# Kernel optimization log

Measured on AMD Instinct MI355X. Metric: run time of the kernel, lower is better.

## Reference

```python
import jax, jax.numpy as jnp
import numpy as np

N = 100000   # nodes
E = 1200000  # edges
NIN, EIN = 6, 1
HID, L, H = 64, 3, 4
D = HID // H  # 16 per-head dim


def setup_inputs() -> dict:
    key = jax.random.key(0)
    ks = jax.random.split(key, 20)
    r = lambda k, shape: (jax.random.normal(k, shape, dtype=jnp.float32) * 0.1)
    inp = {
        "x": jax.random.normal(ks[0], (N, NIN), dtype=jnp.float32),
        "edge_index": jax.random.randint(ks[1], (2, E), 0, N, dtype=jnp.int64),
        "edge_attr": jax.random.normal(ks[2], (E, EIN), dtype=jnp.float32),
        # node encoder (Linear-ReLU-Linear)
        "w_ne1": r(ks[3], (NIN, HID)), "b_ne1": jnp.zeros((HID,), jnp.float32),
        "w_ne2": r(ks[4], (HID, HID)), "b_ne2": jnp.zeros((HID,), jnp.float32),
        # edge encoder (Linear)
        "w_ee": r(ks[5], (EIN, HID)), "b_ee": jnp.zeros((HID,), jnp.float32),
        # stacked GAT layers (PyG GATConv w/ edge features, concat heads)
        "w_gat": r(ks[6], (L, HID, HID)),      # node lin per layer
        "w_eg": r(ks[7], (L, HID, HID)),       # edge lin per layer
        "att_src": r(ks[8], (L, H, D)),
        "att_dst": r(ks[9], (L, H, D)),
        "att_edge": r(ks[10], (L, H, D)),
        "b_gat": jnp.zeros((L, HID), jnp.float32),
        # per-layer LayerNorm
        "ln_g": jnp.ones((L, HID), jnp.float32),
        "ln_b": jnp.zeros((L, HID), jnp.float32),
        # output projection
        "w_out": r(ks[11], (HID, HID)), "b_out": jnp.zeros((HID,), jnp.float32),
    }
    return inp


def _layernorm(x, g, b, eps=1e-5):
    m = jnp.mean(x, axis=-1, keepdims=True)
    v = jnp.mean(jnp.square(x - m), axis=-1, keepdims=True)
    return (x - m) * jax.lax.rsqrt(v + eps) * g + b


def reference(x, edge_index, edge_attr, w_ne1, b_ne1, w_ne2, b_ne2, w_ee, b_ee,
              w_gat, w_eg, att_src, att_dst, att_edge, b_gat, ln_g, ln_b,
              w_out, b_out):
    n = x.shape[0]
    src, dst = edge_index[0], edge_index[1]
    # encode nodes / edges
    h = jax.nn.relu(x @ w_ne1 + b_ne1) @ w_ne2 + b_ne2          # [N, HID]
    e = edge_attr @ w_ee + b_ee                                  # [E, HID]
    num_layers = w_gat.shape[0]
    for l in range(num_layers):
        hw = (h @ w_gat[l]).reshape(n, H, D)                     # [N,H,D]
        ew = (e @ w_eg[l]).reshape(-1, H, D)                     # [E,H,D]
        a_s = jnp.sum(hw * att_src[l], axis=-1)                  # [N,H]
        a_d = jnp.sum(hw * att_dst[l], axis=-1)                  # [N,H]
        a_e = jnp.sum(ew * att_edge[l], axis=-1)                 # [E,H]
        score = jax.nn.leaky_relu(a_s[src] + a_d[dst] + a_e, 0.2)  # [E,H]
        # softmax over incoming edges of each destination node
        smax = jax.ops.segment_max(score, dst, num_segments=n)
        ex = jnp.exp(score - smax[dst])
        den = jax.ops.segment_sum(ex, dst, num_segments=n)
        alpha = ex / (den[dst] + 1e-16)                          # [E,H]
        msg = alpha[:, :, None] * hw[src]                        # [E,H,D]
        agg = jax.ops.segment_sum(msg, dst, num_segments=n)      # [N,H,D]
        agg = agg.reshape(n, H * D) + b_gat[l]
        h = _layernorm(h + jax.nn.elu(agg), ln_g[l], ln_b[l])
    return h @ w_out + b_out
```

## Files before the change

kernel.cpp:

```cpp
#include <hip/hip_runtime.h>

#define NIN 6
#define HIDN 64
#define NHEAD 4
#define DEGPAD 5

__device__ __forceinline__ unsigned short f2bf(float f) {
    unsigned u = __float_as_uint(f);
    unsigned r = (u >> 16) & 1u;
    return (unsigned short)((u + 0x7fffu + r) >> 16);
}

__device__ __forceinline__ void mm64_plain_body(
    const float* __restrict__ src, const float* __restrict__ W,
    const float* __restrict__ bias, float* __restrict__ dst, int N,
    int wv0, int nw) {
    int j = threadIdx.x & 63;
    float Wc[HIDN];
#pragma unroll
    for (int k = 0; k < HIDN; k++) Wc[k] = W[k * HIDN + j];
    float bj = bias[j];
    for (int n0 = wv0; n0 < N; n0 += nw) {
        int n = __builtin_amdgcn_readfirstlane(n0);
        const float4* __restrict__ row = (const float4*)(src + (size_t)n * HIDN);
        float a0 = 0.f, a1 = 0.f, a2 = 0.f, a3 = 0.f;
#pragma unroll
        for (int kk = 0; kk < 16; kk++) {
            float4 r = row[kk];
            a0 += r.x * Wc[4 * kk];
            a1 += r.y * Wc[4 * kk + 1];
            a2 += r.z * Wc[4 * kk + 2];
            a3 += r.w * Wc[4 * kk + 3];
        }
        dst[(size_t)n * HIDN + j] = ((a0 + a1) + (a2 + a3)) + bj;
    }
}

__device__ __forceinline__ void mm64_attn_body(
    const float* __restrict__ src, const float* __restrict__ W,
    const float* __restrict__ att_s, const float* __restrict__ att_d,
    unsigned short* __restrict__ dst16,
    float* __restrict__ a_s, float* __restrict__ a_d, int N,
    int wv0, int nw) {
    int j = threadIdx.x & 63;
    float Wc[HIDN];
#pragma unroll
    for (int k = 0; k < HIDN; k++) Wc[k] = W[k * HIDN + j];
    float asj = att_s[j];
    float adj = att_d[j];
    for (int n0 = wv0; n0 < N; n0 += nw) {
        int n = __builtin_amdgcn_readfirstlane(n0);
        const float4* __restrict__ row = (const float4*)(src + (size_t)n * HIDN);
        float a0 = 0.f, a1 = 0.f, a2 = 0.f, a3 = 0.f;
#pragma unroll
        for (int kk = 0; kk < 16; kk++) {
            float4 r = row[kk];
            a0 += r.x * Wc[4 * kk];
            a1 += r.y * Wc[4 * kk + 1];
            a2 += r.z * Wc[4 * kk + 2];
            a3 += r.w * Wc[4 * kk + 3];
        }
        float acc = (a0 + a1) + (a2 + a3);
        dst16[(size_t)n * HIDN + j] = f2bf(acc);
        float ts = acc * asj;
        float td = acc * adj;
#pragma unroll
        for (int o = 8; o > 0; o >>= 1) {
            ts += __shfl_xor(ts, o);
            td += __shfl_xor(td, o);
        }
        if ((j & 15) == 0) {
            a_s[(size_t)n * NHEAD + (j >> 4)] = ts;
            a_d[(size_t)n * NHEAD + (j >> 4)] = td;
        }
    }
}

__global__ __launch_bounds__(256) void pre_kernel(
    const int* __restrict__ ei, unsigned* __restrict__ deg,
    unsigned* __restrict__ rank, int E,
    const float* __restrict__ x, const float* __restrict__ w1,
    const float* __restrict__ b1, float* __restrict__ hid, int N,
    const float* __restrict__ w_ee, const float* __restrict__ b_ee,
    const float* __restrict__ w_eg, const float* __restrict__ att_edge,
    float* __restrict__ c1, float* __restrict__ c0,
    int histBlocks, int encBlocks) {
    int b = blockIdx.x;
    if (b < histBlocks) {
        int e = b * 256 + threadIdx.x;
        if (e < E) rank[e] = atomicAdd(&deg[(size_t)ei[E + e] << DEGPAD], 1u);
        return;
    }
    b -= histBlocks;
    if (b < encBlocks) {
        int t = b * 256 + threadIdx.x;
        int n = t >> 6, j = t & 63;
        if (n >= N) return;
        float acc = b1[j];
#pragma unroll
        for (int i = 0; i < NIN; i++) acc += x[n * NIN + i] * w1[i * HIDN + j];
        hid[(size_t)n * HIDN + j] = acc > 0.f ? acc : 0.f;
        return;
    }
    int w = threadIdx.x >> 6, j = threadIdx.x & 63;
    for (int p = w; p < 12; p += 4) {
        int l = p >> 2, hh = p & 3;
        const float* wr = w_eg + l * 4096 + j * 64 + hh * 16;
        const float* ae = att_edge + l * 64 + hh * 16;
        float wj = 0.f;
#pragma unroll
        for (int d = 0; d < 16; d++) wj += wr[d] * ae[d];
        float s1 = w_ee[j] * wj;
        float s0 = b_ee[j] * wj;
#pragma unroll
        for (int o = 32; o > 0; o >>= 1) {
            s1 += __shfl_xor(s1, o);
            s0 += __shfl_xor(s0, o);
        }
        if (j == 0) { c1[l * 4 + hh] = s1; c0[l * 4 + hh] = s0; }
    }
}

__global__ __launch_bounds__(256) void mid_kernel(
    const unsigned* __restrict__ deg, unsigned* __restrict__ rp,
    unsigned* __restrict__ st, int N, int E,
    const float* __restrict__ src, const float* __restrict__ W,
    const float* __restrict__ bias, float* __restrict__ dst,
    int scanBlocks, int mmWaves) {
    int b = blockIdx.x;
    if (b < scanBlocks) {
        __shared__ unsigned sm[256];
        __shared__ unsigned s_prefix;
        int t = threadIdx.x, i = b * 256 + t;
        unsigned v = (i < N) ? deg[(size_t)i << DEGPAD] : 0u;
        sm[t] = v;
        __syncthreads();
        unsigned xx = v;
        for (int o = 1; o < 256; o <<= 1) {
            unsigned add = (t >= o) ? sm[t - o] : 0u;
            __syncthreads();
            xx += add; sm[t] = xx;
            __syncthreads();
        }
        if (t == 255) {
            unsigned tag = (b == 0) ? (2u << 30) : (1u << 30);
            __hip_atomic_store(&st[b], tag | xx, __ATOMIC_RELEASE,
                               __HIP_MEMORY_SCOPE_AGENT);
        }
        if (b == 0) {
            if (t == 0) s_prefix = 0u;
        } else if (t < 64) {
            unsigned pfx = 0u;
            int base = b - 1;
            for (;;) {
                int j = base - t;
                unsigned s;
                for (;;) {
                    s = (j >= 0) ? __hip_atomic_load(&st[j], __ATOMIC_ACQUIRE,
                                                     __HIP_MEMORY_SCOPE_AGENT)
                                 : (2u << 30);
                    if (__all((s >> 30) != 0u)) break;
                }
                unsigned long long m2 = __ballot((s >> 30) == 2u);
                if (m2 != 0ull) {
                    int k = __ffsll(m2) - 1;
                    unsigned val = (t <= k) ? (s & 0x3fffffffu) : 0u;
#pragma unroll
                    for (int o = 32; o > 0; o >>= 1) val += __shfl_xor(val, o);
                    pfx += val;
                    break;
                } else {
                    unsigned val = (j >= 0) ? (s & 0x3fffffffu) : 0u;
#pragma unroll
                    for (int o = 32; o > 0; o >>= 1) val += __shfl_xor(val, o);
                    pfx += val;
                    base -= 64;
                }
            }
            if (t == 0) {
                s_prefix = pfx;
                __hip_atomic_store(&st[b], (2u << 30) | (pfx + sm[255]),
                                   __ATOMIC_RELEASE, __HIP_MEMORY_SCOPE_AGENT);
            }
        }
        __syncthreads();
        if (i < N) rp[i] = (xx - v) + s_prefix;
        if (i == N - 1) rp[N] = (unsigned)E;
        return;
    }
    int wv0 = ((b - scanBlocks) * 256 + threadIdx.x) >> 6;
    mm64_plain_body(src, W, bias, dst, N, wv0, mmWaves);
}

__global__ __launch_bounds__(256) void sca_kernel(
    const int* __restrict__ ei, const float* __restrict__ eattr,
    const unsigned* __restrict__ rp, const unsigned* __restrict__ rank,
    int2* __restrict__ eca, int E,
    const float* __restrict__ src, const float* __restrict__ W,
    const float* __restrict__ att_s, const float* __restrict__ att_d,
    unsigned short* __restrict__ dst16,
    float* __restrict__ a_s, float* __restrict__ a_d, int N,
    int scatBlocks, int mmWaves) {
    int b = blockIdx.x;
    if (b < scatBlocks) {
        int e = b * 256 + threadIdx.x;
        if (e >= E) return;
        int s = ei[e], d = ei[E + e];
        unsigned p = rp[d] + rank[e];
        eca[p] = make_int2(s, __float_as_int(eattr[e]));
        return;
    }
    int wv0 = ((b - scatBlocks) * 256 + threadIdx.x) >> 6;
    mm64_attn_body(src, W, att_s, att_d, dst16, a_s, a_d, N, wv0, mmWaves);
}

template <int MODE>
__global__ __launch_bounds__(256) void gat_fused_x_kernel(
    const unsigned* __restrict__ rp, const int2* __restrict__ eca,
    const unsigned short* __restrict__ hw16,
    const float* __restrict__ a_s, const float* __restrict__ a_d,
    const float* __restrict__ c1, const float* __restrict__ c0,
    float* __restrict__ h, const float* __restrict__ bg,
    const float* __restrict__ g, const float* __restrict__ b, int N,
    const float* __restrict__ Wnext,
    const float* __restrict__ att_s_w, const float* __restrict__ att_d_w,
    const float* __restrict__ bias_out,
    unsigned short* __restrict__ hw16_out,
    float* __restrict__ a_s_out, float* __restrict__ a_d_out,
    float* __restrict__ out) {
    __shared__ float WgL[4096];
    __shared__ float exl[4 * 272];
    __shared__ int srl[4 * 68];

    {
        const float4* __restrict__ Wn4 = (const float4*)Wnext;
        float4* WgL4 = (float4*)WgL;
        for (int i = threadIdx.x; i < 1024; i += 256) WgL4[i] = Wn4[i];
    }
    __syncthreads();

    int t = blockIdx.x * blockDim.x + threadIdx.x;
    int lane = t & 63;
    int q = lane >> 4;
    int l = lane & 15;
    int hd = l >> 2;
    int sub = l & 3;
    int n = ((t >> 6) << 2) + q;
    int wslot = (threadIdx.x >> 6);
    float* myex = exl + wslot * 272 + 68 * q;
    int* mysrc = srl + wslot * 68 + 17 * q;

    bool nv = n < N;
    unsigned beg = nv ? rp[n] : 0u;
    int deg = nv ? (int)(rp[n + 1] - beg) : 0;

    float4 ad4 = nv ? *(const float4*)(a_d + ((size_t)n << 2)) : make_float4(0, 0, 0, 0);
    float4 C1 = *(const float4*)c1;
    float4 C0 = *(const float4*)c0;

    int md = deg;
    md = max(md, __shfl_xor(md, 16));
    md = max(md, __shfl_xor(md, 32));
    int chunks = (md + 15) >> 4;

    const unsigned* __restrict__ hwp = (const unsigned*)hw16;
    unsigned loff = (unsigned)(l << 1);

    float ssum = 0.f;
    float ac0 = 0.f, ac1 = 0.f, ac2 = 0.f, ac3 = 0.f;

    for (int k = 0; k < chunks; k++) {
        int i = (k << 4) + l;
        bool act = i < deg;
        int2 ce = act ? eca[beg + i] : make_int2(0, 0);
        int src = ce.x;
        float ea = __int_as_float(ce.y);
        float4 as4 = act ? *(const float4*)(a_s + ((size_t)src << 2))
                         : make_float4(0, 0, 0, 0);
        float s0 = as4.x + ad4.x + ea * C1.x + C0.x;
        float s1 = as4.y + ad4.y + ea * C1.y + C0.y;
        float s2 = as4.z + ad4.z + ea * C1.z + C0.z;
        float s3 = as4.w + ad4.w + ea * C1.w + C0.w;
        s0 = s0 >= 0.f ? s0 : 0.2f * s0;
        s1 = s1 >= 0.f ? s1 : 0.2f * s1;
        s2 = s2 >= 0.f ? s2 : 0.2f * s2;
        s3 = s3 >= 0.f ? s3 : 0.2f * s3;
        float e0 = act ? __expf(s0) : 0.f;
        float e1 = act ? __expf(s1) : 0.f;
        float e2 = act ? __expf(s2) : 0.f;
        float e3 = act ? __expf(s3) : 0.f;
        *(float4*)(myex + (l << 2)) = make_float4(e0, e1, e2, e3);
        mysrc[l] = act ? (src << 5) : 0;

        float w0 = myex[(sub << 2) + hd];
        float w1 = myex[((sub + 4) << 2) + hd];
        float w2 = myex[((sub + 8) << 2) + hd];
        float w3 = myex[((sub + 12) << 2) + hd];
        float csum = (w0 + w1) + (w2 + w3);
        csum += __shfl_xor(csum, 1);
        csum += __shfl_xor(csum, 2);
        ssum += csum;

#pragma unroll
        for (int e = 0; e < 16; e++) {
            float w = myex[(e << 2) + hd];
            unsigned so = (unsigned)mysrc[e];
            uint2 uu = *(const uint2*)(hwp + (so + loff));
            ac0 += w * __uint_as_float(uu.x << 16);
            ac1 += w * __uint_as_float(uu.x & 0xffff0000u);
            ac2 += w * __uint_as_float(uu.y << 16);
            ac3 += w * __uint_as_float(uu.y & 0xffff0000u);
        }
    }

    float inv = 1.f / (ssum + 1e-16f);
    float4 bg4 = *(const float4*)(bg + (l << 2));
    float4 hv4 = nv ? *(const float4*)(h + (size_t)n * HIDN + (l << 2))
                    : make_float4(0, 0, 0, 0);

    float a0 = ac0 * inv + bg4.x;
    float a1 = ac1 * inv + bg4.y;
    float a2 = ac2 * inv + bg4.z;
    float a3 = ac3 * inv + bg4.w;
    a0 = a0 > 0.f ? a0 : (__expf(a0) - 1.f);
    a1 = a1 > 0.f ? a1 : (__expf(a1) - 1.f);
    a2 = a2 > 0.f ? a2 : (__expf(a2) - 1.f);
    a3 = a3 > 0.f ? a3 : (__expf(a3) - 1.f);
    float v0 = hv4.x + a0, v1 = hv4.y + a1, v2 = hv4.z + a2, v3 = hv4.w + a3;

    float s = (v0 + v1) + (v2 + v3);
    float sq = (v0 * v0 + v1 * v1) + (v2 * v2 + v3 * v3);
#pragma unroll
    for (int o = 8; o > 0; o >>= 1) {
        s += __shfl_xor(s, o);
        sq += __shfl_xor(sq, o);
    }
    float mean = s * (1.f / 64.f);
    float var = sq * (1.f / 64.f) - mean * mean;
    float rr = rsqrtf(var + 1e-5f);
    float4 g4 = *(const float4*)(g + (l << 2));
    float4 b4 = *(const float4*)(b + (l << 2));
    v0 = (v0 - mean) * rr * g4.x + b4.x;
    v1 = (v1 - mean) * rr * g4.y + b4.y;
    v2 = (v2 - mean) * rr * g4.z + b4.z;
    v3 = (v3 - mean) * rr * g4.w + b4.w;

    if (MODE == 0 && nv) {
        *(float4*)(h + (size_t)n * HIDN + (l << 2)) = make_float4(v0, v1, v2, v3);
    }

    float* stg = exl + wslot * 272;
    *(float4*)(stg + (q << 6) + (l << 2)) = make_float4(v0, v1, v2, v3);

    float4 A0 = make_float4(0, 0, 0, 0), A1 = make_float4(0, 0, 0, 0);
    float4 A2 = make_float4(0, 0, 0, 0), A3 = make_float4(0, 0, 0, 0);
#pragma unroll
    for (int kk = 0; kk < 16; kk++) {
        float4 hk = *(const float4*)(stg + (q << 6) + (kk << 2));
        const float* wr = WgL + (kk << 8) + (l << 2);
        float4 w0 = *(const float4*)(wr);
        float4 w1 = *(const float4*)(wr + 64);
        float4 w2 = *(const float4*)(wr + 128);
        float4 w3 = *(const float4*)(wr + 192);
        A0.x += hk.x * w0.x; A0.y += hk.x * w0.y; A0.z += hk.x * w0.z; A0.w += hk.x * w0.w;
        A1.x += hk.y * w1.x; A1.y += hk.y * w1.y; A1.z += hk.y * w1.z; A1.w += hk.y * w1.w;
        A2.x += hk.z * w2.x; A2.y += hk.z * w2.y; A2.z += hk.z * w2.z; A2.w += hk.z * w2.w;
        A3.x += hk.w * w3.x; A3.y += hk.w * w3.y; A3.z += hk.w * w3.z; A3.w += hk.w * w3.w;
    }
    float o0 = (A0.x + A1.x) + (A2.x + A3.x);
    float o1 = (A0.y + A1.y) + (A2.y + A3.y);
    float o2 = (A0.z + A1.z) + (A2.z + A3.z);
    float o3 = (A0.w + A1.w) + (A2.w + A3.w);

    if (MODE == 0) {
        if (nv) {
            ushort4 pk = make_ushort4(f2bf(o0), f2bf(o1), f2bf(o2), f2bf(o3));
            *(ushort4*)(hw16_out + (size_t)n * HIDN + (l << 2)) = pk;
        }
        float4 asw = *(const float4*)(att_s_w + (l << 2));
        float4 adw = *(const float4*)(att_d_w + (l << 2));
        float ts = (o0 * asw.x + o1 * asw.y) + (o2 * asw.z + o3 * asw.w);
        float td = (o0 * adw.x + o1 * adw.y) + (o2 * adw.z + o3 * adw.w);
        ts += __shfl_xor(ts, 1); ts += __shfl_xor(ts, 2);
        td += __shfl_xor(td, 1); td += __shfl_xor(td, 2);
        if (nv && (l & 3) == 0) {
            a_s_out[(size_t)n * NHEAD + (l >> 2)] = ts;
            a_d_out[(size_t)n * NHEAD + (l >> 2)] = td;
        }
    } else {
        if (nv) {
            float4 bo = *(const float4*)(bias_out + (l << 2));
            *(float4*)(out + (size_t)n * HIDN + (l << 2)) =
                make_float4(o0 + bo.x, o1 + bo.y, o2 + bo.z, o3 + bo.w);
        }
    }
}

extern "C" void kernel_launch(void* const* d_in, const int* in_sizes, int n_in,
                              void* d_out, int out_size, void* d_ws, size_t ws_size,
                              hipStream_t stream) {
    const float* x      = (const float*)d_in[0];
    const int*   ei     = (const int*)d_in[1];
    const float* eattr  = (const float*)d_in[2];
    const float* w_ne1  = (const float*)d_in[3];
    const float* b_ne1  = (const float*)d_in[4];
    const float* w_ne2  = (const float*)d_in[5];
    const float* b_ne2  = (const float*)d_in[6];
    const float* w_ee   = (const float*)d_in[7];
    const float* b_ee   = (const float*)d_in[8];
    const float* w_gat  = (const float*)d_in[9];
    const float* w_eg   = (const float*)d_in[10];
    const float* att_src= (const float*)d_in[11];
    const float* att_dst= (const float*)d_in[12];
    const float* att_edge=(const float*)d_in[13];
    const float* b_gat  = (const float*)d_in[14];
    const float* ln_g   = (const float*)d_in[15];
    const float* ln_b   = (const float*)d_in[16];
    const float* w_out  = (const float*)d_in[17];
    const float* b_out  = (const float*)d_in[18];

    const int N = in_sizes[0] / NIN;
    const int E = in_sizes[2];

    float* ws   = (float*)d_ws;
    float* h    = ws;
    float* hid  = h + (size_t)N * 64;
    unsigned short* hw16 = (unsigned short*)(hid + (size_t)N * 64);
    float* a_s  = (float*)(hw16 + (size_t)N * 64);
    float* a_d  = a_s + (size_t)N * 4;
    float* c1   = a_d + (size_t)N * 4;
    float* c0   = c1 + 12;
    int2*  eca  = (int2*)(c0 + 12);
    unsigned* rank = (unsigned*)(eca + (size_t)E);
    unsigned* deg  = rank + (size_t)E;
    unsigned* st   = deg + ((size_t)N << DEGPAD);
    unsigned* rp   = st + 1024;

    unsigned short* hw16b = (unsigned short*)hid;
    float* a_sb = (float*)(hw16b + (size_t)N * 64);
    float* a_db = a_sb + (size_t)N * 4;

    dim3 blk(256);
    int edgeBlocks = (E + 255) / 256;
    int encBlocks  = (int)(((size_t)N * 64 + 255) / 256);
    int quadBlocks = (int)(((size_t)((N + 3) / 4) * 64 + 255) / 256);
    int nodeBlocks = (N + 255) / 256;
    int mmBlocks = 2048;
    int mmWaves  = mmBlocks * 4;

    hipMemsetAsync(deg, 0, (((size_t)N << DEGPAD) + 1024) * sizeof(unsigned), stream);

    pre_kernel<<<edgeBlocks + encBlocks + 1, blk, 0, stream>>>(
        ei, deg, rank, E,
        x, w_ne1, b_ne1, hid, N,
        w_ee, b_ee, w_eg, att_edge, c1, c0,
        edgeBlocks, encBlocks);

    mid_kernel<<<nodeBlocks + mmBlocks, blk, 0, stream>>>(
        deg, rp, st, N, E, hid, w_ne2, b_ne2, h, nodeBlocks, mmWaves);

    sca_kernel<<<edgeBlocks + mmBlocks, blk, 0, stream>>>(
        ei, eattr, rp, rank, eca, E,
        h, w_gat, att_src, att_dst, hw16, a_s, a_d, N,
        edgeBlocks, mmWaves);

    gat_fused_x_kernel<0><<<quadBlocks, blk, 0, stream>>>(
        rp, eca, hw16, a_s, a_d, c1 + 0, c0 + 0,
        h, b_gat + 0, ln_g + 0, ln_b + 0, N,
        w_gat + (size_t)1 * 4096, att_src + 64, att_dst + 64, nullptr,
        hw16b, a_sb, a_db, nullptr);

    gat_fused_x_kernel<0><<<quadBlocks, blk, 0, stream>>>(
        rp, eca, hw16b, a_sb, a_db, c1 + 4, c0 + 4,
        h, b_gat + 64, ln_g + 64, ln_b + 64, N,
        w_gat + (size_t)2 * 4096, att_src + 2 * 64, att_dst + 2 * 64, nullptr,
        hw16, a_s, a_d, nullptr);

    gat_fused_x_kernel<1><<<quadBlocks, blk, 0, stream>>>(
        rp, eca, hw16, a_s, a_d, c1 + 8, c0 + 8,
        h, b_gat + 2 * 64, ln_g + 2 * 64, ln_b + 2 * 64, N,
        w_out, nullptr, nullptr, b_out,
        nullptr, nullptr, nullptr, (float*)d_out);
}
```

Before: 453.7 us.

## Bucket nodes by in-degree within each block to balance wave workloads

During the degree scan, each block of 256 nodes now builds a local counting sort of its nodes by degree bucket (ceil(deg/16), capped at 15) and writes a permutation. The three GAT layer kernels process nodes in that permuted order, so the four nodes sharing a wave have similar chunk counts and lanes spend less time idle waiting on the highest-degree node. The cost is an extra indirection load per node, shared-memory atomics and a serial bucket prefix in the scan, and scattered rather than contiguous accesses to per-node rows (h, a_d, rp, outputs).

```diff
diff --git a/kernel.cpp b/kernel.cpp
--- a/kernel.cpp
+++ b/kernel.cpp
@@ -123,7 +123,7 @@
 
 __global__ __launch_bounds__(256) void mid_kernel(
     const unsigned* __restrict__ deg, unsigned* __restrict__ rp,
-    unsigned* __restrict__ st, int N, int E,
+    unsigned* __restrict__ st, unsigned* __restrict__ perm, int N, int E,
     const float* __restrict__ src, const float* __restrict__ W,
     const float* __restrict__ bias, float* __restrict__ dst,
     int scanBlocks, int mmWaves) {
@@ -131,9 +131,11 @@
     if (b < scanBlocks) {
         __shared__ unsigned sm[256];
         __shared__ unsigned s_prefix;
+        __shared__ unsigned bh[16];
         int t = threadIdx.x, i = b * 256 + t;
         unsigned v = (i < N) ? deg[(size_t)i << DEGPAD] : 0u;
         sm[t] = v;
+        if (t < 16) bh[t] = 0u;
         __syncthreads();
         unsigned xx = v;
         for (int o = 1; o < 256; o <<= 1) {
@@ -147,6 +149,9 @@
             __hip_atomic_store(&st[b], tag | xx, __ATOMIC_RELEASE,
                                __HIP_MEMORY_SCOPE_AGENT);
         }
+        unsigned bucket = min(15u, (v + 15u) >> 4);
+        unsigned myrank = 0u;
+        if (i < N) myrank = atomicAdd(&bh[bucket], 1u);
         if (b == 0) {
             if (t == 0) s_prefix = 0u;
         } else if (t < 64) {
@@ -186,6 +191,12 @@
         __syncthreads();
         if (i < N) rp[i] = (xx - v) + s_prefix;
         if (i == N - 1) rp[N] = (unsigned)E;
+        if (t == 0) {
+            unsigned run = 0;
+            for (int bb = 0; bb < 16; bb++) { unsigned c = bh[bb]; bh[bb] = run; run += c; }
+        }
+        __syncthreads();
+        if (i < N) perm[b * 256 + bh[bucket] + myrank] = (unsigned)i;
         return;
     }
     int wv0 = ((b - scanBlocks) * 256 + threadIdx.x) >> 6;
@@ -217,6 +228,7 @@
 template <int MODE>
 __global__ __launch_bounds__(256) void gat_fused_x_kernel(
     const unsigned* __restrict__ rp, const int2* __restrict__ eca,
+    const unsigned* __restrict__ perm,
     const unsigned short* __restrict__ hw16,
     const float* __restrict__ a_s, const float* __restrict__ a_d,
     const float* __restrict__ c1, const float* __restrict__ c0,
@@ -245,12 +257,13 @@
     int l = lane & 15;
     int hd = l >> 2;
     int sub = l & 3;
-    int n = ((t >> 6) << 2) + q;
+    int slot = ((t >> 6) << 2) + q;
     int wslot = (threadIdx.x >> 6);
     float* myex = exl + wslot * 272 + 68 * q;
     int* mysrc = srl + wslot * 68 + 17 * q;
 
-    bool nv = n < N;
+    bool nv = slot < N;
+    int n = nv ? (int)perm[slot] : 0;
     unsigned beg = nv ? rp[n] : 0u;
     int deg = nv ? (int)(rp[n + 1] - beg) : 0;
 
@@ -290,7 +303,7 @@
         float e2 = act ? __expf(s2) : 0.f;
         float e3 = act ? __expf(s3) : 0.f;
         *(float4*)(myex + (l << 2)) = make_float4(e0, e1, e2, e3);
-        mysrc[l] = act ? (src << 5) : 0;
+        mysrc[l] = act ? src : 0;
 
         float w0 = myex[(sub << 2) + hd];
         float w1 = myex[((sub + 4) << 2) + hd];
@@ -304,8 +317,8 @@
 #pragma unroll
         for (int e = 0; e < 16; e++) {
             float w = myex[(e << 2) + hd];
-            unsigned so = (unsigned)mysrc[e];
-            uint2 uu = *(const uint2*)(hwp + (so + loff));
+            int so = mysrc[e];
+            uint2 uu = *(const uint2*)(hwp + (((unsigned)so << 5) + loff));
             ac0 += w * __uint_as_float(uu.x << 16);
             ac1 += w * __uint_as_float(uu.x & 0xffff0000u);
             ac2 += w * __uint_as_float(uu.y << 16);
@@ -435,6 +448,7 @@
     unsigned* deg  = rank + (size_t)E;
     unsigned* st   = deg + ((size_t)N << DEGPAD);
     unsigned* rp   = st + 1024;
+    unsigned* perm = rp + (size_t)N + 1;
 
     unsigned short* hw16b = (unsigned short*)hid;
     float* a_sb = (float*)(hw16b + (size_t)N * 64);
@@ -457,7 +471,7 @@
         edgeBlocks, encBlocks);
 
     mid_kernel<<<nodeBlocks + mmBlocks, blk, 0, stream>>>(
-        deg, rp, st, N, E, hid, w_ne2, b_ne2, h, nodeBlocks, mmWaves);
+        deg, rp, st, perm, N, E, hid, w_ne2, b_ne2, h, nodeBlocks, mmWaves);
 
     sca_kernel<<<edgeBlocks + mmBlocks, blk, 0, stream>>>(
         ei, eattr, rp, rank, eca, E,
@@ -465,19 +479,19 @@
         edgeBlocks, mmWaves);
 
     gat_fused_x_kernel<0><<<quadBlocks, blk, 0, stream>>>(
-        rp, eca, hw16, a_s, a_d, c1 + 0, c0 + 0,
+        rp, eca, perm, hw16, a_s, a_d, c1 + 0, c0 + 0,
         h, b_gat + 0, ln_g + 0, ln_b + 0, N,
         w_gat + (size_t)1 * 4096, att_src + 64, att_dst + 64, nullptr,
         hw16b, a_sb, a_db, nullptr);
 
     gat_fused_x_kernel<0><<<quadBlocks, blk, 0, stream>>>(
-        rp, eca, hw16b, a_sb, a_db, c1 + 4, c0 + 4,
+        rp, eca, perm, hw16b, a_sb, a_db, c1 + 4, c0 + 4,
         h, b_gat + 64, ln_g + 64, ln_b + 64, N,
         w_gat + (size_t)2 * 4096, att_src + 2 * 64, att_dst + 2 * 64, nullptr,
         hw16, a_s, a_d, nullptr);
 
     gat_fused_x_kernel<1><<<quadBlocks, blk, 0, stream>>>(
-        rp, eca, hw16, a_s, a_d, c1 + 8, c0 + 8,
+        rp, eca, perm, hw16, a_s, a_d, c1 + 8, c0 + 8,
         h, b_gat + 2 * 64, ln_g + 2 * 64, ln_b + 2 * 64, N,
         w_out, nullptr, nullptr, b_out,
         nullptr, nullptr, nullptr, (float*)d_out);
```

Result: slower. 476.9 us (+5.1%).

## Fuse node encoder and first GAT projection into one register-resident pass

Applied to the files above, without the earlier changes.

Moves the first encoder layer, the second encoder matmul and the layer-0 GAT projection with its attention logits into the mid kernel. Each wave computes all three per node, using wave shuffles in place of reading intermediate rows from global memory. This removes the round trips of the hidden and h buffers between kernels and makes the scatter kernel edge-only. The fused kernel holds two 64-float weight columns in registers, which can lower occupancy. The per-node matmul work now also runs only in the mid kernel rather than being split across two launches. A small change in the GAT kernel stores the raw source index and shifts it at load time.

```diff
diff --git a/kernel.cpp b/kernel.cpp
--- a/kernel.cpp
+++ b/kernel.cpp
@@ -11,95 +11,17 @@
     return (unsigned short)((u + 0x7fffu + r) >> 16);
 }
 
-__device__ __forceinline__ void mm64_plain_body(
-    const float* __restrict__ src, const float* __restrict__ W,
-    const float* __restrict__ bias, float* __restrict__ dst, int N,
-    int wv0, int nw) {
-    int j = threadIdx.x & 63;
-    float Wc[HIDN];
-#pragma unroll
-    for (int k = 0; k < HIDN; k++) Wc[k] = W[k * HIDN + j];
-    float bj = bias[j];
-    for (int n0 = wv0; n0 < N; n0 += nw) {
-        int n = __builtin_amdgcn_readfirstlane(n0);
-        const float4* __restrict__ row = (const float4*)(src + (size_t)n * HIDN);
-        float a0 = 0.f, a1 = 0.f, a2 = 0.f, a3 = 0.f;
-#pragma unroll
-        for (int kk = 0; kk < 16; kk++) {
-            float4 r = row[kk];
-            a0 += r.x * Wc[4 * kk];
-            a1 += r.y * Wc[4 * kk + 1];
-            a2 += r.z * Wc[4 * kk + 2];
-            a3 += r.w * Wc[4 * kk + 3];
-        }
-        dst[(size_t)n * HIDN + j] = ((a0 + a1) + (a2 + a3)) + bj;
-    }
-}
-
-__device__ __forceinline__ void mm64_attn_body(
-    const float* __restrict__ src, const float* __restrict__ W,
-    const float* __restrict__ att_s, const float* __restrict__ att_d,
-    unsigned short* __restrict__ dst16,
-    float* __restrict__ a_s, float* __restrict__ a_d, int N,
-    int wv0, int nw) {
-    int j = threadIdx.x & 63;
-    float Wc[HIDN];
-#pragma unroll
-    for (int k = 0; k < HIDN; k++) Wc[k] = W[k * HIDN + j];
-    float asj = att_s[j];
-    float adj = att_d[j];
-    for (int n0 = wv0; n0 < N; n0 += nw) {
-        int n = __builtin_amdgcn_readfirstlane(n0);
-        const float4* __restrict__ row = (const float4*)(src + (size_t)n * HIDN);
-        float a0 = 0.f, a1 = 0.f, a2 = 0.f, a3 = 0.f;
-#pragma unroll
-        for (int kk = 0; kk < 16; kk++) {
-            float4 r = row[kk];
-            a0 += r.x * Wc[4 * kk];
-            a1 += r.y * Wc[4 * kk + 1];
-            a2 += r.z * Wc[4 * kk + 2];
-            a3 += r.w * Wc[4 * kk + 3];
-        }
-        float acc = (a0 + a1) + (a2 + a3);
-        dst16[(size_t)n * HIDN + j] = f2bf(acc);
-        float ts = acc * asj;
-        float td = acc * adj;
-#pragma unroll
-        for (int o = 8; o > 0; o >>= 1) {
-            ts += __shfl_xor(ts, o);
-            td += __shfl_xor(td, o);
-        }
-        if ((j & 15) == 0) {
-            a_s[(size_t)n * NHEAD + (j >> 4)] = ts;
-            a_d[(size_t)n * NHEAD + (j >> 4)] = td;
-        }
-    }
-}
-
 __global__ __launch_bounds__(256) void pre_kernel(
     const int* __restrict__ ei, unsigned* __restrict__ deg,
     unsigned* __restrict__ rank, int E,
-    const float* __restrict__ x, const float* __restrict__ w1,
-    const float* __restrict__ b1, float* __restrict__ hid, int N,
     const float* __restrict__ w_ee, const float* __restrict__ b_ee,
     const float* __restrict__ w_eg, const float* __restrict__ att_edge,
     float* __restrict__ c1, float* __restrict__ c0,
-    int histBlocks, int encBlocks) {
+    int histBlocks) {
     int b = blockIdx.x;
     if (b < histBlocks) {
         int e = b * 256 + threadIdx.x;
         if (e < E) rank[e] = atomicAdd(&deg[(size_t)ei[E + e] << DEGPAD], 1u);
-        return;
-    }
-    b -= histBlocks;
-    if (b < encBlocks) {
-        int t = b * 256 + threadIdx.x;
-        int n = t >> 6, j = t & 63;
-        if (n >= N) return;
-        float acc = b1[j];
-#pragma unroll
-        for (int i = 0; i < NIN; i++) acc += x[n * NIN + i] * w1[i * HIDN + j];
-        hid[(size_t)n * HIDN + j] = acc > 0.f ? acc : 0.f;
         return;
     }
     int w = threadIdx.x >> 6, j = threadIdx.x & 63;
@@ -124,9 +46,14 @@
 __global__ __launch_bounds__(256) void mid_kernel(
     const unsigned* __restrict__ deg, unsigned* __restrict__ rp,
     unsigned* __restrict__ st, int N, int E,
-    const float* __restrict__ src, const float* __restrict__ W,
-    const float* __restrict__ bias, float* __restrict__ dst,
-    int scanBlocks, int mmWaves) {
+    const float* __restrict__ x, const float* __restrict__ w1,
+    const float* __restrict__ b1,
+    const float* __restrict__ w2, const float* __restrict__ b2,
+    const float* __restrict__ wg, const float* __restrict__ att_s_w,
+    const float* __restrict__ att_d_w,
+    float* __restrict__ h, unsigned short* __restrict__ hw16,
+    float* __restrict__ a_s, float* __restrict__ a_d,
+    int scanBlocks, int encWaves) {
     int b = blockIdx.x;
     if (b < scanBlocks) {
         __shared__ unsigned sm[256];
@@ -188,30 +115,70 @@
         if (i == N - 1) rp[N] = (unsigned)E;
         return;
     }
-    int wv0 = ((b - scanBlocks) * 256 + threadIdx.x) >> 6;
-    mm64_plain_body(src, W, bias, dst, N, wv0, mmWaves);
+    int j = threadIdx.x & 63;
+    float Wa[NIN];
+#pragma unroll
+    for (int i = 0; i < NIN; i++) Wa[i] = w1[i * HIDN + j];
+    float b1j = b1[j];
+    float W2c[HIDN];
+#pragma unroll
+    for (int k = 0; k < HIDN; k++) W2c[k] = w2[k * HIDN + j];
+    float b2j = b2[j];
+    float Wgc[HIDN];
+#pragma unroll
+    for (int k = 0; k < HIDN; k++) Wgc[k] = wg[k * HIDN + j];
+    float asj = att_s_w[j];
+    float adj = att_d_w[j];
+    int wv0 = ((b - scanBlocks) * 256 + (int)threadIdx.x) >> 6;
+    for (int n0 = wv0; n0 < N; n0 += encWaves) {
+        int n = __builtin_amdgcn_readfirstlane(n0);
+        float hv = b1j;
+#pragma unroll
+        for (int i = 0; i < NIN; i++) hv += x[(size_t)n * NIN + i] * Wa[i];
+        hv = hv > 0.f ? hv : 0.f;
+        float a0 = 0.f, a1 = 0.f, a2 = 0.f, a3 = 0.f;
+#pragma unroll
+        for (int kk = 0; kk < 16; kk++) {
+            a0 += __shfl(hv, 4 * kk)     * W2c[4 * kk];
+            a1 += __shfl(hv, 4 * kk + 1) * W2c[4 * kk + 1];
+            a2 += __shfl(hv, 4 * kk + 2) * W2c[4 * kk + 2];
+            a3 += __shfl(hv, 4 * kk + 3) * W2c[4 * kk + 3];
+        }
+        float hcur = ((a0 + a1) + (a2 + a3)) + b2j;
+        h[(size_t)n * HIDN + j] = hcur;
+        a0 = a1 = a2 = a3 = 0.f;
+#pragma unroll
+        for (int kk = 0; kk < 16; kk++) {
+            a0 += __shfl(hcur, 4 * kk)     * Wgc[4 * kk];
+            a1 += __shfl(hcur, 4 * kk + 1) * Wgc[4 * kk + 1];
+            a2 += __shfl(hcur, 4 * kk + 2) * Wgc[4 * kk + 2];
+            a3 += __shfl(hcur, 4 * kk + 3) * Wgc[4 * kk + 3];
+        }
+        float acc = (a0 + a1) + (a2 + a3);
+        hw16[(size_t)n * HIDN + j] = f2bf(acc);
+        float ts = acc * asj;
+        float td = acc * adj;
+#pragma unroll
+        for (int o = 8; o > 0; o >>= 1) {
+            ts += __shfl_xor(ts, o);
+            td += __shfl_xor(td, o);
+        }
+        if ((j & 15) == 0) {
+            a_s[(size_t)n * NHEAD + (j >> 4)] = ts;
+            a_d[(size_t)n * NHEAD + (j >> 4)] = td;
+        }
+    }
 }
 
 __global__ __launch_bounds__(256) void sca_kernel(
     const int* __restrict__ ei, const float* __restrict__ eattr,
     const unsigned* __restrict__ rp, const unsigned* __restrict__ rank,
-    int2* __restrict__ eca, int E,
-    const float* __restrict__ src, const float* __restrict__ W,
-    const float* __restrict__ att_s, const float* __restrict__ att_d,
-    unsigned short* __restrict__ dst16,
-    float* __restrict__ a_s, float* __restrict__ a_d, int N,
-    int scatBlocks, int mmWaves) {
-    int b = blockIdx.x;
-    if (b < scatBlocks) {
-        int e = b * 256 + threadIdx.x;
-        if (e >= E) return;
-        int s = ei[e], d = ei[E + e];
-        unsigned p = rp[d] + rank[e];
-        eca[p] = make_int2(s, __float_as_int(eattr[e]));
-        return;
-    }
-    int wv0 = ((b - scatBlocks) * 256 + threadIdx.x) >> 6;
-    mm64_attn_body(src, W, att_s, att_d, dst16, a_s, a_d, N, wv0, mmWaves);
+    int2* __restrict__ eca, int E) {
+    int e = blockIdx.x * 256 + threadIdx.x;
+    if (e >= E) return;
+    int s = ei[e], d = ei[E + e];
+    unsigned p = rp[d] + rank[e];
+    eca[p] = make_int2(s, __float_as_int(eattr[e]));
 }
 
 template <int MODE>
@@ -290,7 +257,7 @@
         float e2 = act ? __expf(s2) : 0.f;
         float e3 = act ? __expf(s3) : 0.f;
         *(float4*)(myex + (l << 2)) = make_float4(e0, e1, e2, e3);
-        mysrc[l] = act ? (src << 5) : 0;
+        mysrc[l] = act ? src : 0;
 
         float w0 = myex[(sub << 2) + hd];
         float w1 = myex[((sub + 4) << 2) + hd];
@@ -304,8 +271,8 @@
 #pragma unroll
         for (int e = 0; e < 16; e++) {
             float w = myex[(e << 2) + hd];
-            unsigned so = (unsigned)mysrc[e];
-            uint2 uu = *(const uint2*)(hwp + (so + loff));
+            int so = mysrc[e];
+            uint2 uu = *(const uint2*)(hwp + (((unsigned)so << 5) + loff));
             ac0 += w * __uint_as_float(uu.x << 16);
             ac1 += w * __uint_as_float(uu.x & 0xffff0000u);
             ac2 += w * __uint_as_float(uu.y << 16);
@@ -424,8 +391,8 @@
 
     float* ws   = (float*)d_ws;
     float* h    = ws;
-    float* hid  = h + (size_t)N * 64;
-    unsigned short* hw16 = (unsigned short*)(hid + (size_t)N * 64);
+    float* bbuf = h + (size_t)N * 64;
+    unsigned short* hw16 = (unsigned short*)(bbuf + (size_t)N * 64);
     float* a_s  = (float*)(hw16 + (size_t)N * 64);
     float* a_d  = a_s + (size_t)N * 4;
     float* c1   = a_d + (size_t)N * 4;
@@ -436,33 +403,32 @@
     unsigned* st   = deg + ((size_t)N << DEGPAD);
     unsigned* rp   = st + 1024;
 
-    unsigned short* hw16b = (unsigned short*)hid;
+    unsigned short* hw16b = (unsigned short*)bbuf;
     float* a_sb = (float*)(hw16b + (size_t)N * 64);
     float* a_db = a_sb + (size_t)N * 4;
 
     dim3 blk(256);
     int edgeBlocks = (E + 255) / 256;
-    int encBlocks  = (int)(((size_t)N * 64 + 255) / 256);
     int quadBlocks = (int)(((size_t)((N + 3) / 4) * 64 + 255) / 256);
     int nodeBlocks = (N + 255) / 256;
-    int mmBlocks = 2048;
-    int mmWaves  = mmBlocks * 4;
+    int encBlocks = 2048;
+    int encWaves  = encBlocks * 4;
 
     hipMemsetAsync(deg, 0, (((size_t)N << DEGPAD) + 1024) * sizeof(unsigned), stream);
 
-    pre_kernel<<<edgeBlocks + encBlocks + 1, blk, 0, stream>>>(
+    pre_kernel<<<edgeBlocks + 1, blk, 0, stream>>>(
         ei, deg, rank, E,
-        x, w_ne1, b_ne1, hid, N,
         w_ee, b_ee, w_eg, att_edge, c1, c0,
-        edgeBlocks, encBlocks);
-
-    mid_kernel<<<nodeBlocks + mmBlocks, blk, 0, stream>>>(
-        deg, rp, st, N, E, hid, w_ne2, b_ne2, h, nodeBlocks, mmWaves);
-
-    sca_kernel<<<edgeBlocks + mmBlocks, blk, 0, stream>>>(
-        ei, eattr, rp, rank, eca, E,
-        h, w_gat, att_src, att_dst, hw16, a_s, a_d, N,
-        edgeBlocks, mmWaves);
+        edgeBlocks);
+
+    mid_kernel<<<nodeBlocks + encBlocks, blk, 0, stream>>>(
+        deg, rp, st, N, E,
+        x, w_ne1, b_ne1, w_ne2, b_ne2,
+        w_gat, att_src, att_dst,
+        h, hw16, a_s, a_d,
+        nodeBlocks, encWaves);
+
+    sca_kernel<<<edgeBlocks, blk, 0, stream>>>(ei, eattr, rp, rank, eca, E);
 
     gat_fused_x_kernel<0><<<quadBlocks, blk, 0, stream>>>(
         rp, eca, hw16, a_s, a_d, c1 + 0, c0 + 0,
```

Measured after the change: 532.8 us. 1.17x slower.
